# Kernel tuning notes

Hardware: AMD Instinct MI355X
Metric: run time of the kernel (lower is better)

## Reference

```python
import jax, jax.numpy as jnp
import numpy as np

B, NVIS, NHID, NCLASS = 2048, 2048, 1024, 64


def setup_inputs() -> dict:
    key = jax.random.key(0)
    k1, k2, k3, k4, k5 = jax.random.split(key, 5)
    return {
        "v": jax.random.normal(k1, (B, NVIS), dtype=jnp.float32),
        "W": jax.random.normal(k2, (NVIS, NHID), dtype=jnp.float32),
        "c": jax.random.normal(k3, (1, NHID), dtype=jnp.float32),
        "d": jax.random.normal(k4, (1, NCLASS), dtype=jnp.float32),
        "U": jax.random.normal(k5, (NCLASS, NHID), dtype=jnp.float32),
    }


def reference(v, W, c, d, U):
    # precomputed_factor: [B, nhid]
    pre = jnp.matmul(v, W) + c
    # class free energies F[b, y] = d[0, y] + sum_j softplus(pre[b, j] + U[y, j])
    # broadcast to [B, nclass, nhid], reduce over hidden units
    F = d[0] + jnp.sum(jax.nn.softplus(pre[:, None, :] + U[None, :, :]), axis=-1)  # [B, nclass]
    # pairwise normalization 1 / sum_d exp(F_d - F_c) == softmax(F) along classes
    class_probs = jax.nn.softmax(F, axis=1)
    max_idx = jnp.argmax(class_probs, axis=1)
    one_hot = jax.nn.one_hot(max_idx, U.shape[0], dtype=jnp.int32)
    return class_probs, one_hot
```

## Files before the change

kernel.cpp:

```cpp
#include <hip/hip_runtime.h>

constexpr int kB    = 2048;
constexpr int kVIS  = 2048;
constexpr int kHID  = 1024;
constexpr int kCLS  = 64;
constexpr float kLog2e = 1.4426950408889634f;

typedef __attribute__((ext_vector_type(8))) short bf16x8;
typedef __attribute__((ext_vector_type(4))) float f32x4;

typedef __attribute__((address_space(3))) unsigned       as3_u32;
typedef __attribute__((address_space(1))) const unsigned as1_u32;

__device__ __forceinline__ void g2lds16(const void* g, void* l) {
    __builtin_amdgcn_global_load_lds((as1_u32*)g, (as3_u32*)l, 16, 0, 0);
}

__device__ __forceinline__ unsigned short f2bf(float x) {
    unsigned u = __float_as_uint(x);
    u += 0x7fffu + ((u >> 16) & 1u);
    return (unsigned short)(u >> 16);
}
__device__ __forceinline__ float bf2f(unsigned short h) {
    return __uint_as_float(((unsigned)h) << 16);
}

__global__ __launch_bounds__(256) void prep_all(const float* __restrict__ v,
                                                const float* __restrict__ W,
                                                const float* __restrict__ U,
                                                unsigned short* __restrict__ vh,
                                                unsigned short* __restrict__ vl,
                                                unsigned short* __restrict__ wth,
                                                unsigned short* __restrict__ wtl,
                                                float* __restrict__ Ut) {
    __shared__ float T[32][33];
    const int bx = blockIdx.x;
    if (bx < 4096) {
        const int i = (bx * 256 + threadIdx.x) * 4;
        const float4 xv = *(const float4*)(v + i);
        ushort4 h, l;
        h.x = f2bf(xv.x); l.x = f2bf(xv.x - bf2f(h.x));
        h.y = f2bf(xv.y); l.y = f2bf(xv.y - bf2f(h.y));
        h.z = f2bf(xv.z); l.z = f2bf(xv.z - bf2f(h.z));
        h.w = f2bf(xv.w); l.w = f2bf(xv.w - bf2f(h.w));
        *(ushort4*)(vh + i) = h;
        *(ushort4*)(vl + i) = l;
    } else if (bx < 6144) {
        const int b = bx - 4096;
        const int n0 = (b & 31) * 32, k0 = (b >> 5) * 32;
        const int c = threadIdx.x & 31, r0 = threadIdx.x >> 5;
#pragma unroll
        for (int p = 0; p < 4; ++p) {
            const int r = r0 + p * 8;
            T[r][c] = W[(size_t)(k0 + r) * kHID + n0 + c];
        }
        __syncthreads();
#pragma unroll
        for (int p = 0; p < 4; ++p) {
            const int rr = r0 + p * 8;
            const float x = T[c][rr];
            const unsigned short h = f2bf(x);
            const unsigned short l = f2bf(x - bf2f(h));
            const size_t o = (size_t)(n0 + rr) * kVIS + k0 + c;
            wth[o] = h;
            wtl[o] = l;
        }
    } else {
        const int id = (bx - 6144) * 256 + threadIdx.x;
        const int j = id >> 6, y = id & 63;
        Ut[id] = U[(size_t)y * kHID + j] * kLog2e;
    }
}

__global__ __launch_bounds__(256) void gemm_fused(const unsigned short* __restrict__ vh,
                                                  const unsigned short* __restrict__ vl,
                                                  const unsigned short* __restrict__ wth,
                                                  const unsigned short* __restrict__ wtl,
                                                  const float* __restrict__ cvec,
                                                  const float* __restrict__ Ut,
                                                  float* __restrict__ Fpart) {
    __shared__ __align__(16) union SMem {
        unsigned short stage[4][64 * 64];
        float ps[64][68];
    } smem;
    unsigned short* Ah = smem.stage[0];
    unsigned short* Al = smem.stage[1];
    unsigned short* Bh = smem.stage[2];
    unsigned short* Bl = smem.stage[3];

    const int tid = threadIdx.x;
    const int lane = tid & 63, wave = tid >> 6;
    const int m0 = blockIdx.y * 64, n0 = blockIdx.x * 64;
    const int wm = (wave >> 1) * 32, wn = (wave & 1) * 32;

    const int r0 = tid >> 3, r1 = r0 + 32;
    const int oc = (((tid & 7) ^ ((tid >> 3) & 7)) << 3);
    const size_t ga0 = (size_t)(m0 + r0) * kVIS + oc;
    const size_t ga1 = (size_t)(m0 + r1) * kVIS + oc;
    const size_t gb0 = (size_t)(n0 + r0) * kVIS + oc;
    const size_t gb1 = (size_t)(n0 + r1) * kVIS + oc;
    const int l0 = (r0 << 6) + ((tid & 7) << 3);
    const int l1 = (r1 << 6) + ((tid & 7) << 3);

    const int fm = lane & 15, fq = lane >> 4;
    const int rx = fm & 7;
    const int a0r = (wm + fm) << 6,  a1r = (wm + 16 + fm) << 6;
    const int b0r = (wn + fm) << 6,  b1r = (wn + 16 + fm) << 6;

    f32x4 acc[2][2] = {};

    for (int k0 = 0; k0 < kVIS; k0 += 64) {
        __syncthreads();
        g2lds16(vh + ga0 + k0, Ah + l0);
        g2lds16(vh + ga1 + k0, Ah + l1);
        g2lds16(vl + ga0 + k0, Al + l0);
        g2lds16(vl + ga1 + k0, Al + l1);
        g2lds16(wth + gb0 + k0, Bh + l0);
        g2lds16(wth + gb1 + k0, Bh + l1);
        g2lds16(wtl + gb0 + k0, Bl + l0);
        g2lds16(wtl + gb1 + k0, Bl + l1);
        __syncthreads();
#pragma unroll
        for (int kk = 0; kk < 64; kk += 32) {
            const int p = (((kk >> 3) + fq) ^ rx) << 3;
            const bf16x8 ah0 = *(const bf16x8*)(Ah + a0r + p);
            const bf16x8 ah1 = *(const bf16x8*)(Ah + a1r + p);
            const bf16x8 al0 = *(const bf16x8*)(Al + a0r + p);
            const bf16x8 al1 = *(const bf16x8*)(Al + a1r + p);
            const bf16x8 bh0 = *(const bf16x8*)(Bh + b0r + p);
            const bf16x8 bh1 = *(const bf16x8*)(Bh + b1r + p);
            const bf16x8 bl0 = *(const bf16x8*)(Bl + b0r + p);
            const bf16x8 bl1 = *(const bf16x8*)(Bl + b1r + p);
            acc[0][0] = __builtin_amdgcn_mfma_f32_16x16x32_bf16(ah0, bh0, acc[0][0], 0, 0, 0);
            acc[0][0] = __builtin_amdgcn_mfma_f32_16x16x32_bf16(ah0, bl0, acc[0][0], 0, 0, 0);
            acc[0][0] = __builtin_amdgcn_mfma_f32_16x16x32_bf16(al0, bh0, acc[0][0], 0, 0, 0);
            acc[0][1] = __builtin_amdgcn_mfma_f32_16x16x32_bf16(ah0, bh1, acc[0][1], 0, 0, 0);
            acc[0][1] = __builtin_amdgcn_mfma_f32_16x16x32_bf16(ah0, bl1, acc[0][1], 0, 0, 0);
            acc[0][1] = __builtin_amdgcn_mfma_f32_16x16x32_bf16(al0, bh1, acc[0][1], 0, 0, 0);
            acc[1][0] = __builtin_amdgcn_mfma_f32_16x16x32_bf16(ah1, bh0, acc[1][0], 0, 0, 0);
            acc[1][0] = __builtin_amdgcn_mfma_f32_16x16x32_bf16(ah1, bl0, acc[1][0], 0, 0, 0);
            acc[1][0] = __builtin_amdgcn_mfma_f32_16x16x32_bf16(al1, bh0, acc[1][0], 0, 0, 0);
            acc[1][1] = __builtin_amdgcn_mfma_f32_16x16x32_bf16(ah1, bh1, acc[1][1], 0, 0, 0);
            acc[1][1] = __builtin_amdgcn_mfma_f32_16x16x32_bf16(ah1, bl1, acc[1][1], 0, 0, 0);
            acc[1][1] = __builtin_amdgcn_mfma_f32_16x16x32_bf16(al1, bh1, acc[1][1], 0, 0, 0);
        }
    }

    __syncthreads();
#pragma unroll
    for (int j = 0; j < 2; ++j) {
        const int col = wn + j * 16 + fm;
        const float cv = cvec[n0 + col];
#pragma unroll
        for (int i = 0; i < 2; ++i) {
            const int rbase = wm + i * 16 + fq * 4;
#pragma unroll
            for (int r = 0; r < 4; ++r)
                smem.ps[rbase + r][col] = (acc[i][j][r] + cv) * kLog2e;
        }
    }
    __syncthreads();

    const float* UtN = Ut + (size_t)n0 * kCLS;
    float relu[16], prod[16];
#pragma unroll
    for (int rr = 0; rr < 16; ++rr) { relu[rr] = 0.f; prod[rr] = 1.f; }

    for (int jc = 0; jc < 64; jc += 8) {
        float u[8];
#pragma unroll
        for (int q = 0; q < 8; ++q) u[q] = UtN[(jc + q) * kCLS + lane];
#pragma unroll
        for (int rr = 0; rr < 16; ++rr) {
            const float4 p0 = *(const float4*)&smem.ps[wave * 16 + rr][jc];
            const float4 p1 = *(const float4*)&smem.ps[wave * 16 + rr][jc + 4];
            const float pv[8] = {p0.x, p0.y, p0.z, p0.w, p1.x, p1.y, p1.z, p1.w};
#pragma unroll
            for (int q = 0; q < 8; ++q) {
                const float t = pv[q] + u[q];
                const float e = __builtin_amdgcn_exp2f(-fabsf(t));
                prod[rr] = __builtin_fmaf(prod[rr], e, prod[rr]);
                relu[rr] += fmaxf(t, 0.f);
            }
        }
    }
#pragma unroll
    for (int rr = 0; rr < 16; ++rr) {
        const float contrib = relu[rr] + __builtin_amdgcn_logf(prod[rr]);
        Fpart[((size_t)blockIdx.x * kB + m0 + wave * 16 + rr) * kCLS + lane] = contrib;
    }
}

__global__ __launch_bounds__(256) void softmax_final(const float* __restrict__ Fpart,
                                                     const float* __restrict__ dvec,
                                                     float* __restrict__ out) {
    const int tid = threadIdx.x;
    const int lane = tid & 63, wave = tid >> 6;
    const int row = blockIdx.x * 4 + wave;
    double s = 0.0;
#pragma unroll
    for (int k = 0; k < kHID / 64; ++k)
        s += (double)Fpart[((size_t)k * kB + row) * kCLS + lane];
    const float G = (float)s + dvec[lane] * kLog2e;

    float m = G;
    int mi = lane;
#pragma unroll
    for (int off = 32; off; off >>= 1) {
        const float om = __shfl_xor(m, off);
        const int   oi = __shfl_xor(mi, off);
        if (om > m || (om == m && oi < mi)) { m = om; mi = oi; }
    }
    const float e2 = __builtin_amdgcn_exp2f(G - m);
    float ssum = e2;
#pragma unroll
    for (int off = 32; off; off >>= 1) ssum += __shfl_xor(ssum, off);
    out[(size_t)row * kCLS + lane] = e2 / ssum;
    out[(size_t)kB * kCLS + (size_t)row * kCLS + lane] = (lane == mi) ? 1.0f : 0.0f;
}

constexpr int BM = 64, BN = 64, BK = 16;

__global__ __launch_bounds__(256) void gemm_vw(const float* __restrict__ V,
                                               const float* __restrict__ Wm,
                                               const float* __restrict__ cvec,
                                               float* __restrict__ pre) {
    __shared__ float As[BK][BM + 4];
    __shared__ float Bs[BK][BN + 4];
    const int tid = threadIdx.x;
    const int tx = tid & 15, ty = tid >> 4;
    const int m0 = blockIdx.y * BM, n0 = blockIdx.x * BN;
    const int arow = tid >> 2, acol = (tid & 3) << 2;
    const int brow = tid >> 4, bcol = (tid & 15) << 2;
    const float* vptr = V + (size_t)(m0 + arow) * kVIS + acol;
    const float* wptr = Wm + (size_t)brow * kHID + n0 + bcol;
    float acc[4][4] = {};
    for (int k0 = 0; k0 < kVIS; k0 += BK) {
        const float4 a4 = *(const float4*)(vptr + k0);
        const float4 b4 = *(const float4*)(wptr + (size_t)k0 * kHID);
        __syncthreads();
        As[acol + 0][arow] = a4.x; As[acol + 1][arow] = a4.y;
        As[acol + 2][arow] = a4.z; As[acol + 3][arow] = a4.w;
        *(float4*)&Bs[brow][bcol] = b4;
        __syncthreads();
#pragma unroll
        for (int k = 0; k < BK; ++k) {
            const float4 av = *(const float4*)&As[k][ty << 2];
            const float4 bv = *(const float4*)&Bs[k][tx << 2];
            const float a[4] = {av.x, av.y, av.z, av.w};
            const float b[4] = {bv.x, bv.y, bv.z, bv.w};
#pragma unroll
            for (int i = 0; i < 4; ++i)
#pragma unroll
                for (int j = 0; j < 4; ++j) acc[i][j] += a[i] * b[j];
        }
    }
#pragma unroll
    for (int i = 0; i < 4; ++i) {
        const int row = m0 + (ty << 2) + i;
        const int col = n0 + (tx << 2);
        const float4 cv = *(const float4*)(cvec + col);
        float4 o;
        o.x = acc[i][0] + cv.x; o.y = acc[i][1] + cv.y;
        o.z = acc[i][2] + cv.z; o.w = acc[i][3] + cv.w;
        *(float4*)(pre + (size_t)row * kHID + col) = o;
    }
}

__device__ __forceinline__ float softplus_f(float x) {
    return fmaxf(x, 0.f) + __logf(1.f + __expf(-fabsf(x)));
}

__global__ __launch_bounds__(256) void classify(const float* __restrict__ pre,
                                                const float* __restrict__ U,
                                                const float* __restrict__ dvec,
                                                float* __restrict__ out) {
    __shared__ float preS[4][kHID];
    __shared__ float Fs[4][kCLS];
    const int tid = threadIdx.x;
    const int lane = tid & 63, wave = tid >> 6;
    const int b0 = blockIdx.x * 4;
    const float4* src = (const float4*)(pre + (size_t)b0 * kHID);
    float4* dst = (float4*)preS;
    for (int i = tid; i < kHID; i += 256) dst[i] = src[i];
    __syncthreads();
    for (int yi = 0; yi < 16; ++yi) {
        const int y = (wave << 4) + yi;
        const float* Uy = U + (size_t)y * kHID;
        float a0 = 0.f, a1 = 0.f, a2 = 0.f, a3 = 0.f;
#pragma unroll
        for (int it = 0; it < kHID / 64; ++it) {
            const int j = lane + (it << 6);
            const float u = Uy[j];
            a0 += softplus_f(preS[0][j] + u);
            a1 += softplus_f(preS[1][j] + u);
            a2 += softplus_f(preS[2][j] + u);
            a3 += softplus_f(preS[3][j] + u);
        }
        double d0 = a0, d1 = a1, d2 = a2, d3 = a3;
#pragma unroll
        for (int off = 32; off; off >>= 1) {
            d0 += __shfl_xor(d0, off); d1 += __shfl_xor(d1, off);
            d2 += __shfl_xor(d2, off); d3 += __shfl_xor(d3, off);
        }
        if (lane == 0) {
            const float dy = dvec[y];
            Fs[0][y] = (float)d0 + dy; Fs[1][y] = (float)d1 + dy;
            Fs[2][y] = (float)d2 + dy; Fs[3][y] = (float)d3 + dy;
        }
    }
    __syncthreads();
    const float F = Fs[wave][lane];
    float m = F; int mi = lane;
#pragma unroll
    for (int off = 32; off; off >>= 1) {
        const float om = __shfl_xor(m, off);
        const int oi = __shfl_xor(mi, off);
        if (om > m || (om == m && oi < mi)) { m = om; mi = oi; }
    }
    const float e = __expf(F - m);
    float s = e;
#pragma unroll
    for (int off = 32; off; off >>= 1) s += __shfl_xor(s, off);
    const int row = b0 + wave;
    out[(size_t)row * kCLS + lane] = e / s;
    out[(size_t)kB * kCLS + (size_t)row * kCLS + lane] = (lane == mi) ? 1.0f : 0.0f;
}

extern "C" void kernel_launch(void* const* d_in, const int* in_sizes, int n_in,
                              void* d_out, int out_size, void* d_ws, size_t ws_size,
                              hipStream_t stream) {
    const float* v = (const float*)d_in[0];
    const float* W = (const float*)d_in[1];
    const float* c = (const float*)d_in[2];
    const float* d = (const float*)d_in[3];
    const float* U = (const float*)d_in[4];
    float* out = (float*)d_out;
    char* ws = (char*)d_ws;

    const size_t need = 33816576;
    if (ws_size >= need) {
        unsigned short* vh  = (unsigned short*)(ws);
        unsigned short* vl  = (unsigned short*)(ws + 8388608);
        unsigned short* wth = (unsigned short*)(ws + 16777216);
        unsigned short* wtl = (unsigned short*)(ws + 20971520);
        float* Ut    = (float*)(ws + 25165824);
        float* Fpart = (float*)(ws + 25427968);
        prep_all<<<6400, 256, 0, stream>>>(v, W, U, vh, vl, wth, wtl, Ut);
        gemm_fused<<<dim3(kHID / 64, kB / 64), 256, 0, stream>>>(vh, vl, wth, wtl, c, Ut, Fpart);
        softmax_final<<<kB / 4, 256, 0, stream>>>(Fpart, d, out);
    } else {
        float* pre = (float*)ws;
        gemm_vw<<<dim3(kHID / BN, kB / BM), 256, 0, stream>>>(v, W, c, pre);
        classify<<<kB / 4, 256, 0, stream>>>(pre, U, d, out);
    }
}
```

Baseline: 136.0 us.

## Remap GEMM blocks for XCD locality, pack U as float4, use packed f32x2 epilogue

Replaces the 2D grid with a 1D grid whose block index is remapped so that each group of consecutive blocks shares M stripes, aiming for better L2 reuse across the chiplets. U is relaid out in groups of four hidden units so each lane fetches a float4 instead of four scalar loads. The softplus epilogue now keeps two partial product and relu accumulators per row using f32x2 vectors, so the compiler can emit packed FP32 math and the serial FMA dependency chain is halved. In exchange there are more live registers, and the result is the product of two partial products, which carries a slightly different overflow and rounding behaviour.

```diff
diff --git a/kernel.cpp b/kernel.cpp
--- a/kernel.cpp
+++ b/kernel.cpp
@@ -8,6 +8,7 @@
 
 typedef __attribute__((ext_vector_type(8))) short bf16x8;
 typedef __attribute__((ext_vector_type(4))) float f32x4;
+typedef __attribute__((ext_vector_type(2))) float f32x2;
 
 typedef __attribute__((address_space(3))) unsigned       as3_u32;
 typedef __attribute__((address_space(1))) const unsigned as1_u32;
@@ -32,7 +33,7 @@
                                                 unsigned short* __restrict__ vl,
                                                 unsigned short* __restrict__ wth,
                                                 unsigned short* __restrict__ wtl,
-                                                float* __restrict__ Ut) {
+                                                float* __restrict__ Utp) {
     __shared__ float T[32][33];
     const int bx = blockIdx.x;
     if (bx < 4096) {
@@ -68,7 +69,7 @@
     } else {
         const int id = (bx - 6144) * 256 + threadIdx.x;
         const int j = id >> 6, y = id & 63;
-        Ut[id] = U[(size_t)y * kHID + j] * kLog2e;
+        Utp[(((j >> 2) * kCLS + y) << 2) + (j & 3)] = U[(size_t)y * kHID + j] * kLog2e;
     }
 }
 
@@ -77,7 +78,7 @@
                                                   const unsigned short* __restrict__ wth,
                                                   const unsigned short* __restrict__ wtl,
                                                   const float* __restrict__ cvec,
-                                                  const float* __restrict__ Ut,
+                                                  const float* __restrict__ Utp,
                                                   float* __restrict__ Fpart) {
     __shared__ __align__(16) union SMem {
         unsigned short stage[4][64 * 64];
@@ -90,7 +91,12 @@
 
     const int tid = threadIdx.x;
     const int lane = tid & 63, wave = tid >> 6;
-    const int m0 = blockIdx.y * 64, n0 = blockIdx.x * 64;
+
+    const int bid = blockIdx.x;
+    const int idx = bid >> 3;
+    const int mstripe = ((bid & 7) << 2) + (idx >> 4);
+    const int ncol = idx & 15;
+    const int m0 = mstripe * 64, n0 = ncol * 64;
     const int wm = (wave >> 1) * 32, wn = (wave & 1) * 32;
 
     const int r0 = tid >> 3, r1 = r0 + 32;
@@ -161,33 +167,42 @@
     }
     __syncthreads();
 
-    const float* UtN = Ut + (size_t)n0 * kCLS;
-    float relu[16], prod[16];
-#pragma unroll
-    for (int rr = 0; rr < 16; ++rr) { relu[rr] = 0.f; prod[rr] = 1.f; }
-
+    const int q0 = (n0 >> 2);
+    f32x2 relu2[16], prod2[16];
+#pragma unroll
+    for (int rr = 0; rr < 16; ++rr) { relu2[rr] = (f32x2)(0.f); prod2[rr] = (f32x2)(1.f); }
+
+    const f32x2 zero2 = (f32x2)(0.f);
     for (int jc = 0; jc < 64; jc += 8) {
-        float u[8];
-#pragma unroll
-        for (int q = 0; q < 8; ++q) u[q] = UtN[(jc + q) * kCLS + lane];
+        const float4 ua = ((const float4*)Utp)[(q0 + (jc >> 2) + 0) * kCLS + lane];
+        const float4 ub = ((const float4*)Utp)[(q0 + (jc >> 2) + 1) * kCLS + lane];
+        const f32x2 u01 = {ua.x, ua.y}, u23 = {ua.z, ua.w};
+        const f32x2 u45 = {ub.x, ub.y}, u67 = {ub.z, ub.w};
 #pragma unroll
         for (int rr = 0; rr < 16; ++rr) {
             const float4 p0 = *(const float4*)&smem.ps[wave * 16 + rr][jc];
             const float4 p1 = *(const float4*)&smem.ps[wave * 16 + rr][jc + 4];
-            const float pv[8] = {p0.x, p0.y, p0.z, p0.w, p1.x, p1.y, p1.z, p1.w};
-#pragma unroll
-            for (int q = 0; q < 8; ++q) {
-                const float t = pv[q] + u[q];
-                const float e = __builtin_amdgcn_exp2f(-fabsf(t));
-                prod[rr] = __builtin_fmaf(prod[rr], e, prod[rr]);
-                relu[rr] += fmaxf(t, 0.f);
+            f32x2 tp[4];
+            tp[0] = (f32x2){p0.x, p0.y} + u01;
+            tp[1] = (f32x2){p0.z, p0.w} + u23;
+            tp[2] = (f32x2){p1.x, p1.y} + u45;
+            tp[3] = (f32x2){p1.z, p1.w} + u67;
+#pragma unroll
+            for (int g = 0; g < 4; ++g) {
+                const f32x2 t = tp[g];
+                f32x2 e;
+                e.x = __builtin_amdgcn_exp2f(-__builtin_fabsf(t.x));
+                e.y = __builtin_amdgcn_exp2f(-__builtin_fabsf(t.y));
+                prod2[rr] = __builtin_elementwise_fma(prod2[rr], e, prod2[rr]);
+                relu2[rr] += __builtin_elementwise_max(t, zero2);
             }
         }
     }
 #pragma unroll
     for (int rr = 0; rr < 16; ++rr) {
-        const float contrib = relu[rr] + __builtin_amdgcn_logf(prod[rr]);
-        Fpart[((size_t)blockIdx.x * kB + m0 + wave * 16 + rr) * kCLS + lane] = contrib;
+        const float contrib = relu2[rr].x + relu2[rr].y +
+                              __builtin_amdgcn_logf(prod2[rr].x * prod2[rr].y);
+        Fpart[((size_t)ncol * kB + m0 + wave * 16 + rr) * kCLS + lane] = contrib;
     }
 }
 
@@ -344,10 +359,10 @@
         unsigned short* vl  = (unsigned short*)(ws + 8388608);
         unsigned short* wth = (unsigned short*)(ws + 16777216);
         unsigned short* wtl = (unsigned short*)(ws + 20971520);
-        float* Ut    = (float*)(ws + 25165824);
+        float* Utp   = (float*)(ws + 25165824);
         float* Fpart = (float*)(ws + 25427968);
-        prep_all<<<6400, 256, 0, stream>>>(v, W, U, vh, vl, wth, wtl, Ut);
-        gemm_fused<<<dim3(kHID / 64, kB / 64), 256, 0, stream>>>(vh, vl, wth, wtl, c, Ut, Fpart);
+        prep_all<<<6400, 256, 0, stream>>>(v, W, U, vh, vl, wth, wtl, Utp);
+        gemm_fused<<<512, 256, 0, stream>>>(vh, vl, wth, wtl, c, Utp, Fpart);
         softmax_final<<<kB / 4, 256, 0, stream>>>(Fpart, d, out);
     } else {
         float* pre = (float*)ws;
```

Measured after the change: 131.5 us. -3.3%, faster.
